# Kernel optimization log

Hardware: AMD Instinct MI355X
Metric: run time of the kernel (lower is better)

The kernel has to match this reference:

```python
import jax, jax.numpy as jnp
import numpy as np

N = 2800        # real node count (before hardcoded pad)
NPAD = 3000     # module pads node dim to 3000
F_IN = 8192     # node_features
H1 = 256        # dim_h1 (GCLSTM in_channels)
H2 = 128        # GCLSTM out_channels
E = 179200      # edges (avg degree 64)


def setup_inputs() -> dict:
    key = jax.random.key(0)
    ks = jax.random.split(key, 12)
    inp = {
        "x": jax.random.normal(ks[0], (N, F_IN), jnp.float32),
        "edge_index": jax.random.randint(ks[1], (2, E), 0, N, dtype=jnp.int64),
        "edge_weight": jax.random.uniform(ks[2], (E,), jnp.float32),
        "h0": jax.random.normal(ks[3], (NPAD, H2), jnp.float32),
        "c0": jax.random.normal(ks[4], (NPAD, H2), jnp.float32),
        # fc0: node_features -> dim_h1
        "fc0_w": jax.random.normal(ks[5], (F_IN, H1), jnp.float32) / np.float32(np.sqrt(F_IN)),
        "fc0_b": jnp.zeros((H1,), jnp.float32),
        # GCLSTM gate params, stacked over gates [i, f, c, o]
        "Wx": jax.random.normal(ks[6], (4, H1, H2), jnp.float32) / np.float32(np.sqrt(H1)),
        "bg": jnp.zeros((4, H2), jnp.float32),
        # ChebConv (K=2) weights per gate: theta_0, theta_1, bias
        "cw0": jax.random.normal(ks[7], (4, H2, H2), jnp.float32) / np.float32(np.sqrt(H2)),
        "cw1": jax.random.normal(ks[8], (4, H2, H2), jnp.float32) / np.float32(np.sqrt(H2)),
        "cb": jnp.zeros((4, H2), jnp.float32),
        # final fc: 128 -> 1
        "fc_w": jax.random.normal(ks[9], (H2, 1), jnp.float32) / np.float32(np.sqrt(H2)),
        "fc_b": jnp.zeros((1,), jnp.float32),
    }
    return inp


def _cheb_scaled_laplacian(edge_index, edge_weight, num_nodes):
    # ChebConv 'sym' norm with lambda_max=2: L_hat = -D^{-1/2} A D^{-1/2}
    # (diagonal of scaled Laplacian cancels to zero with fill_value=-1 self loops)
    row, col = edge_index[0], edge_index[1]
    deg = jax.ops.segment_sum(edge_weight, row, num_segments=num_nodes)
    dinv = jnp.where(deg > 0, jax.lax.rsqrt(jnp.where(deg > 0, deg, 1.0)), 0.0)
    return -dinv[row] * edge_weight * dinv[col]  # per-edge weight of L_hat


def reference(x, edge_weight, h0, c0, fc0_w, fc0_b, Wx, bg, cw0, cw1, cb,
              fc_w, fc_b, edge_index):
    n_real = x.shape[0]
    # hardcoded zero-padding of node dim to 3000
    xp = jnp.concatenate([x, jnp.zeros((NPAD - n_real, x.shape[1]), x.dtype)], axis=0)
    z = jax.nn.relu(xp @ fc0_w + fc0_b)                       # [3000, 256]

    row, col = edge_index[0], edge_index[1]
    w_hat = _cheb_scaled_laplacian(edge_index, edge_weight, NPAD)
    # Chebyshev T1 term: L_hat @ H  (shared across all four gates)
    T1 = jax.ops.segment_sum(w_hat[:, None] * h0[row], col, num_segments=NPAD)  # [3000,128]

    # all four gate pre-activations at once: X W_x + ChebConv(H) + b
    gates = (jnp.einsum('nf,gfo->gno', z, Wx)
             + jnp.einsum('nd,gdo->gno', h0, cw0)
             + jnp.einsum('nd,gdo->gno', T1, cw1)
             + (bg + cb)[:, None, :])                          # [4, 3000, 128]

    i = jax.nn.sigmoid(gates[0])
    f = jax.nn.sigmoid(gates[1])
    t = jnp.tanh(gates[2])
    o = jax.nn.sigmoid(gates[3])
    c_new = f * c0 + i * t
    h_new = o * jnp.tanh(c_new)                                # [3000, 128]

    out = (jax.nn.relu(h_new) @ fc_w + fc_b)[:, 0]             # squeeze last dim
    out = out[:n_real]                                         # drop padding rows
    return out, h_new
```

## Files before the change

kernel.cpp:

```cpp
#include <hip/hip_runtime.h>
#include <math.h>

#define N_REAL 2800
#define NPAD   3000
#define F_IN   8192
#define H1     256
#define H2     128
#define NE     179200
#define UDIM   512
#define NGATE  512
#define MPAD   3072
#define SPLITK 16
#define KCH    (F_IN / SPLITK)

typedef _Float16 half8_t __attribute__((ext_vector_type(8)));
typedef _Float16 half4_t __attribute__((ext_vector_type(4)));
typedef float    floatx4 __attribute__((ext_vector_type(4)));

__device__ __forceinline__ void async_g2l_16(const _Float16* g, _Float16* l) {
    __builtin_amdgcn_global_load_lds(
        (const __attribute__((address_space(1))) unsigned int*)g,
        (__attribute__((address_space(3))) unsigned int*)l, 16, 0, 0);
}

__global__ __launch_bounds__(256)
void prep_kernel(const float* __restrict__ w, const float* __restrict__ Wx,
                 const float* __restrict__ cw0, const float* __restrict__ cw1,
                 const float* __restrict__ bg, const float* __restrict__ cb,
                 _Float16* __restrict__ wT, _Float16* __restrict__ Wc,
                 float* __restrict__ biasv) {
    int b = blockIdx.x;
    if (b < 2048) {
        __shared__ float tile[32][33];
        int k0 = (b & 255) * 32;
        int n0 = (b >> 8) * 32;
        int tx = threadIdx.x & 31, ty = threadIdx.x >> 5;
#pragma unroll
        for (int r = 0; r < 4; r++)
            tile[ty + r * 8][tx] = w[(size_t)(k0 + ty + r * 8) * H1 + n0 + tx];
        __syncthreads();
#pragma unroll
        for (int r = 0; r < 4; r++)
            wT[(size_t)(n0 + ty + r * 8) * F_IN + k0 + tx] = (_Float16)tile[tx][ty + r * 8];
    } else {
        int idx = (b - 2048) * 256 + threadIdx.x;
        if (idx < UDIM * NGATE) {
            int col = idx >> 9;
            int f   = idx & 511;
            int g = col >> 7, o = col & 127;
            float v;
            if (f < H1)            v = Wx[((size_t)g * H1 + f) * H2 + o];
            else if (f < H1 + H2)  v = cw0[((size_t)g * H2 + (f - H1)) * H2 + o];
            else                   v = cw1[((size_t)g * H2 + (f - H1 - H2)) * H2 + o];
            Wc[idx] = (_Float16)v;
            if (f == 0) biasv[col] = bg[col] + cb[col];
        }
    }
}

__global__ __launch_bounds__(256, 3)
void gemm1_fused(const float* __restrict__ x, const _Float16* __restrict__ wT,
                 float* __restrict__ P) {
    __shared__ __align__(16) _Float16 As[8][64][8];
    __shared__ __align__(16) _Float16 Bs[8][256][8];
    const int t = threadIdx.x;
    const int wave = t >> 6, lane = t & 63;
    const int l16 = lane & 15, u4 = lane >> 4;
    const int m0 = blockIdx.x * 64;
    const int kbase = blockIdx.y * KCH;

    const int arow = t >> 2;
    const int aseg = t & 3;
    const bool avalid = (m0 + arow) < N_REAL;
    const float* agp = x + (size_t)(m0 + arow) * F_IN + kbase + aseg * 16;

    floatx4 acc[4][4] = {};

    for (int kk = 0; kk < KCH; kk += 64) {
#pragma unroll
        for (int q = 0; q < 2; q++) {
            int u = wave * 2 + q;
            const _Float16* bsrc = wT + kbase + kk + u * 8;
#pragma unroll
            for (int rg = 0; rg < 4; rg++)
                async_g2l_16(bsrc + (size_t)(rg * 64 + lane) * F_IN, &Bs[u][rg * 64 + lane][0]);
        }
        float4 a0 = make_float4(0.f, 0.f, 0.f, 0.f), a1 = a0, a2 = a0, a3 = a0;
        if (avalid) {
            a0 = *(const float4*)(agp + kk);
            a1 = *(const float4*)(agp + kk + 4);
            a2 = *(const float4*)(agp + kk + 8);
            a3 = *(const float4*)(agp + kk + 12);
        }
        half8_t hlo, hhi;
        hlo[0] = (_Float16)a0.x; hlo[1] = (_Float16)a0.y; hlo[2] = (_Float16)a0.z; hlo[3] = (_Float16)a0.w;
        hlo[4] = (_Float16)a1.x; hlo[5] = (_Float16)a1.y; hlo[6] = (_Float16)a1.z; hlo[7] = (_Float16)a1.w;
        hhi[0] = (_Float16)a2.x; hhi[1] = (_Float16)a2.y; hhi[2] = (_Float16)a2.z; hhi[3] = (_Float16)a2.w;
        hhi[4] = (_Float16)a3.x; hhi[5] = (_Float16)a3.y; hhi[6] = (_Float16)a3.z; hhi[7] = (_Float16)a3.w;
        *(half8_t*)&As[aseg * 2][arow][0]     = hlo;
        *(half8_t*)&As[aseg * 2 + 1][arow][0] = hhi;
        __syncthreads();
#pragma unroll
        for (int ks = 0; ks < 2; ks++) {
            half8_t a[4], b[4];
#pragma unroll
            for (int i = 0; i < 4; i++) a[i] = *(const half8_t*)&As[ks * 4 + u4][i * 16 + l16][0];
#pragma unroll
            for (int j = 0; j < 4; j++) b[j] = *(const half8_t*)&Bs[ks * 4 + u4][wave * 64 + j * 16 + l16][0];
#pragma unroll
            for (int i = 0; i < 4; i++)
#pragma unroll
                for (int j = 0; j < 4; j++)
                    acc[i][j] = __builtin_amdgcn_mfma_f32_16x16x32_f16(a[i], b[j], acc[i][j], 0, 0, 0);
        }
        __syncthreads();
    }

    float* Pb = P + ((size_t)blockIdx.y * MPAD + m0) * H1;
#pragma unroll
    for (int i = 0; i < 4; i++)
#pragma unroll
        for (int j = 0; j < 4; j++) {
            int n = wave * 64 + j * 16 + l16;
#pragma unroll
            for (int r = 0; r < 4; r++)
                Pb[(size_t)(i * 16 + u4 * 4 + r) * H1 + n] = acc[i][j][r];
        }
}

__global__ void hist_kernel(const int* __restrict__ ei, const float* __restrict__ ew,
                            float* __restrict__ deg, int* __restrict__ counts) {
    int e = blockIdx.x * blockDim.x + threadIdx.x;
    if (e < NE) {
        int r = ei[e];
        int c = ei[NE + e];
        atomicAdd(&deg[r], ew[e]);
        atomicAdd(&counts[c], 1);
    }
}

__global__ __launch_bounds__(1024)
void scan_kernel(const int* __restrict__ counts, int* __restrict__ offsets,
                 const float* __restrict__ deg, float* __restrict__ dinv,
                 int* __restrict__ cursor) {
    __shared__ int wt[16];
    int t = threadIdx.x;
    int i0 = t * 3;
    int v0 = (i0     < NPAD) ? counts[i0]     : 0;
    int v1 = (i0 + 1 < NPAD) ? counts[i0 + 1] : 0;
    int v2 = (i0 + 2 < NPAD) ? counts[i0 + 2] : 0;
    int s = v0 + v1 + v2;
    int incl = s;
#pragma unroll
    for (int d = 1; d < 64; d <<= 1) {
        int n = __shfl_up(incl, d);
        if ((t & 63) >= d) incl += n;
    }
    if ((t & 63) == 63) wt[t >> 6] = incl;
    __syncthreads();
    if (t < 64) {
        int w = (t < 16) ? wt[t] : 0;
        int wi = w;
#pragma unroll
        for (int d = 1; d < 16; d <<= 1) {
            int n = __shfl_up(wi, d);
            if (t >= d) wi += n;
        }
        if (t < 16) wt[t] = wi - w;
    }
    __syncthreads();
    int base = wt[t >> 6] + (incl - s);
    if (i0 <= NPAD)     { offsets[i0] = base;              if (i0     < NPAD) cursor[i0]     = base; }
    if (i0 + 1 <= NPAD) { offsets[i0 + 1] = base + v0;     if (i0 + 1 < NPAD) cursor[i0 + 1] = base + v0; }
    if (i0 + 2 <= NPAD) { offsets[i0 + 2] = base + v0 + v1; if (i0 + 2 < NPAD) cursor[i0 + 2] = base + v0 + v1; }
    for (int i = t; i < NPAD; i += 1024) {
        float d = deg[i];
        dinv[i] = (d > 0.f) ? rsqrtf(d) : 0.f;
    }
}

__global__ void scatter_kernel(const int* __restrict__ ei, int* __restrict__ cursor,
                               int* __restrict__ eid) {
    int e = blockIdx.x * blockDim.x + threadIdx.x;
    if (e < NE) {
        int c = ei[NE + e];
        int p = atomicAdd(&cursor[c], 1);
        eid[p] = e;
    }
}

#define ZBLK 1536
#define HBLK 768
__global__ __launch_bounds__(128)
void t1epi_kernel(const int* __restrict__ ei, const float* __restrict__ ew,
                  const float* __restrict__ h0, const float* __restrict__ dinv,
                  const int* __restrict__ offsets, const int* __restrict__ eid,
                  const float* __restrict__ P, const float* __restrict__ fc0_b,
                  _Float16* __restrict__ U16) {
    int b = blockIdx.x;
    int t = threadIdx.x;
    if (b < NPAD) {
        __shared__ int   sr[128];
        __shared__ float sw[128];
        int n = b;
        int beg = offsets[n], end = offsets[n + 1];
        float dc = dinv[n];
        float acc = 0.f;
        for (int base = beg; base < end; base += 128) {
            int j = base + t;
            if (j < end) {
                int e = eid[j];
                int r = ei[e];
                sr[t] = r;
                sw[t] = -dinv[r] * ew[e];
            }
            __syncthreads();
            int cnt = min(128, end - base);
            for (int k = 0; k < cnt; k++)
                acc += sw[k] * h0[(size_t)sr[k] * H2 + t];
            __syncthreads();
        }
        U16[(size_t)n * UDIM + H1 + H2 + t] = (_Float16)(acc * dc);
    } else if (b < NPAD + ZBLK) {
        int q = (b - NPAD) * 128 + t;
        int m = q >> 6;
        int n4 = (q & 63) * 4;
        float sx = 0.f, sy = 0.f, sz = 0.f, sw = 0.f;
#pragma unroll
        for (int sk = 0; sk < SPLITK; sk++) {
            float4 p = *(const float4*)&P[((size_t)sk * MPAD + m) * H1 + n4];
            sx += p.x; sy += p.y; sz += p.z; sw += p.w;
        }
        float4 bb = *(const float4*)&fc0_b[n4];
        half4_t h;
        h[0] = (_Float16)fmaxf(sx + bb.x, 0.f);
        h[1] = (_Float16)fmaxf(sy + bb.y, 0.f);
        h[2] = (_Float16)fmaxf(sz + bb.z, 0.f);
        h[3] = (_Float16)fmaxf(sw + bb.w, 0.f);
        *(half4_t*)&U16[(size_t)m * UDIM + n4] = h;
    } else {
        int q = (b - NPAD - ZBLK) * 128 + t;
        int m = q >> 5;
        int o4 = (q & 31) * 4;
        half4_t h = {};
        if (m < NPAD) {
            float4 v = *(const float4*)&h0[(size_t)m * H2 + o4];
            h[0] = (_Float16)v.x; h[1] = (_Float16)v.y; h[2] = (_Float16)v.z; h[3] = (_Float16)v.w;
        }
        *(half4_t*)&U16[(size_t)m * UDIM + H1 + o4] = h;
    }
}

__global__ __launch_bounds__(256, 3)
void gemm2_mfma(const _Float16* __restrict__ U16, const _Float16* __restrict__ Wc,
                float* __restrict__ gates) {
    __shared__ __align__(16) _Float16 As[8][64][8];
    __shared__ __align__(16) _Float16 Bs[8][256][8];
    const int t = threadIdx.x;
    const int wave = t >> 6, lane = t & 63;
    const int l16 = lane & 15, u4 = lane >> 4;
    const int n0 = blockIdx.x * 256;
    const int m0 = blockIdx.y * 64;

    floatx4 acc[4][4] = {};

    for (int kk = 0; kk < UDIM; kk += 64) {
#pragma unroll
        for (int q = 0; q < 2; q++) {
            int u = wave * 2 + q;
            async_g2l_16(U16 + (size_t)(m0 + lane) * UDIM + kk + u * 8, &As[u][lane][0]);
            const _Float16* bsrc = Wc + kk + u * 8;
#pragma unroll
            for (int rg = 0; rg < 4; rg++)
                async_g2l_16(bsrc + (size_t)(n0 + rg * 64 + lane) * UDIM, &Bs[u][rg * 64 + lane][0]);
        }
        __syncthreads();
#pragma unroll
        for (int ks = 0; ks < 2; ks++) {
            half8_t a[4], b[4];
#pragma unroll
            for (int i = 0; i < 4; i++) a[i] = *(const half8_t*)&As[ks * 4 + u4][i * 16 + l16][0];
#pragma unroll
            for (int j = 0; j < 4; j++) b[j] = *(const half8_t*)&Bs[ks * 4 + u4][wave * 64 + j * 16 + l16][0];
#pragma unroll
            for (int i = 0; i < 4; i++)
#pragma unroll
                for (int j = 0; j < 4; j++)
                    acc[i][j] = __builtin_amdgcn_mfma_f32_16x16x32_f16(a[i], b[j], acc[i][j], 0, 0, 0);
        }
        __syncthreads();
    }

#pragma unroll
    for (int i = 0; i < 4; i++)
#pragma unroll
        for (int j = 0; j < 4; j++) {
            int n = n0 + wave * 64 + j * 16 + l16;
#pragma unroll
            for (int r = 0; r < 4; r++)
                gates[(size_t)(m0 + i * 16 + u4 * 4 + r) * NGATE + n] = acc[i][j][r];
        }
}

__global__ __launch_bounds__(128)
void lstm_kernel(const float* __restrict__ gates, const float* __restrict__ c0,
                 const float* __restrict__ biasv, const float* __restrict__ fc_w,
                 const float* __restrict__ fc_b, float* __restrict__ out) {
    __shared__ float red[2];
    int n = blockIdx.x;
    int o = threadIdx.x;
    const float* g = gates + (size_t)n * NGATE;
    float gi = g[o]          + biasv[o];
    float gf = g[H2 + o]     + biasv[H2 + o];
    float gt = g[2 * H2 + o] + biasv[2 * H2 + o];
    float go = g[3 * H2 + o] + biasv[3 * H2 + o];
    float iv = 1.f / (1.f + expf(-gi));
    float fv = 1.f / (1.f + expf(-gf));
    float tv = tanhf(gt);
    float ov = 1.f / (1.f + expf(-go));
    float c = fv * c0[(size_t)n * H2 + o] + iv * tv;
    float h = ov * tanhf(c);
    out[N_REAL + (size_t)n * H2 + o] = h;

    float r = fmaxf(h, 0.f) * fc_w[o];
#pragma unroll
    for (int s = 32; s; s >>= 1) r += __shfl_down(r, s);
    if ((o & 63) == 0) red[o >> 6] = r;
    __syncthreads();
    if (o == 0 && n < N_REAL) out[n] = red[0] + red[1] + fc_b[0];
}

extern "C" void kernel_launch(void* const* d_in, const int* in_sizes, int n_in,
                              void* d_out, int out_size, void* d_ws, size_t ws_size,
                              hipStream_t stream) {
    const float* x     = (const float*)d_in[0];
    const int*   ei    = (const int*)d_in[1];
    const float* ew    = (const float*)d_in[2];
    const float* h0    = (const float*)d_in[3];
    const float* c0    = (const float*)d_in[4];
    const float* fc0_w = (const float*)d_in[5];
    const float* fc0_b = (const float*)d_in[6];
    const float* Wx    = (const float*)d_in[7];
    const float* bg    = (const float*)d_in[8];
    const float* cw0   = (const float*)d_in[9];
    const float* cw1   = (const float*)d_in[10];
    const float* cb    = (const float*)d_in[11];
    const float* fc_w  = (const float*)d_in[12];
    const float* fc_b  = (const float*)d_in[13];
    float* out = (float*)d_out;

    float* P      = (float*)d_ws;
    float* gates  = P + (size_t)SPLITK * MPAD * H1;
    float* biasv  = gates + (size_t)MPAD * NGATE;
    float* deg    = biasv + NGATE;
    float* dinv   = deg + NPAD;
    int*   counts = (int*)(dinv + NPAD);
    int*   offs   = counts + 3072;
    int*   cursor = offs + 3072;
    int*   eid    = cursor + 3072;
    _Float16* U16 = (_Float16*)(((uintptr_t)(eid + NE) + 255) & ~(uintptr_t)255);
    _Float16* Wc  = U16 + (size_t)MPAD * UDIM;
    _Float16* wT  = Wc + (size_t)UDIM * NGATE;

    hipMemsetAsync(deg, 0, NPAD * sizeof(float), stream);
    hipMemsetAsync(counts, 0, 3072 * sizeof(int), stream);

    prep_kernel<<<3072, 256, 0, stream>>>(fc0_w, Wx, cw0, cw1, bg, cb, wT, Wc, biasv);
    gemm1_fused<<<dim3(MPAD / 64, SPLITK), 256, 0, stream>>>(x, wT, P);
    hist_kernel<<<(NE + 255) / 256, 256, 0, stream>>>(ei, ew, deg, counts);
    scan_kernel<<<1, 1024, 0, stream>>>(counts, offs, deg, dinv, cursor);
    scatter_kernel<<<(NE + 255) / 256, 256, 0, stream>>>(ei, cursor, eid);
    t1epi_kernel<<<NPAD + ZBLK + HBLK, 128, 0, stream>>>(ei, ew, h0, dinv, offs, eid, P, fc0_b, U16);
    gemm2_mfma<<<dim3(NGATE / 256, MPAD / 64), 256, 0, stream>>>(U16, Wc, gates);
    lstm_kernel<<<NPAD, 128, 0, stream>>>(gates, c0, biasv, fc_w, fc_b, out);
}
```

Baseline: 295.7 us.

## Store split-K partials in fp16, split gemm2 K, unroll T1 gather, fold memsets

The gemm1 split-K partial sums are now written and read as fp16 instead of fp32, halving the partial-buffer traffic, and gemm1's launch bounds are raised to 4 blocks per SM. gemm2 gets a 2-way K split, writing two partial gate buffers that the LSTM kernel adds together, so it launches twice as many blocks. The T1 neighbour gather is unrolled by 8 to keep more loads in flight. The two memsets are folded into extra prep_kernel blocks to save launches. Rounding partials to fp16 before the reduction adds precision risk.

```diff
diff --git a/kernel.cpp b/kernel.cpp
--- a/kernel.cpp
+++ b/kernel.cpp
@@ -28,7 +28,8 @@
                  const float* __restrict__ cw0, const float* __restrict__ cw1,
                  const float* __restrict__ bg, const float* __restrict__ cb,
                  _Float16* __restrict__ wT, _Float16* __restrict__ Wc,
-                 float* __restrict__ biasv) {
+                 float* __restrict__ biasv, float* __restrict__ deg,
+                 int* __restrict__ counts) {
     int b = blockIdx.x;
     if (b < 2048) {
         __shared__ float tile[32][33];
@@ -42,7 +43,7 @@
 #pragma unroll
         for (int r = 0; r < 4; r++)
             wT[(size_t)(n0 + ty + r * 8) * F_IN + k0 + tx] = (_Float16)tile[tx][ty + r * 8];
-    } else {
+    } else if (b < 3072) {
         int idx = (b - 2048) * 256 + threadIdx.x;
         if (idx < UDIM * NGATE) {
             int col = idx >> 9;
@@ -55,12 +56,16 @@
             Wc[idx] = (_Float16)v;
             if (f == 0) biasv[col] = bg[col] + cb[col];
         }
-    }
-}
-
-__global__ __launch_bounds__(256, 3)
+    } else {
+        int i = (b - 3072) * 256 + threadIdx.x;
+        if (i < NPAD) deg[i] = 0.f;
+        else { int j = i - NPAD; if (j < 3072) counts[j] = 0; }
+    }
+}
+
+__global__ __launch_bounds__(256, 4)
 void gemm1_fused(const float* __restrict__ x, const _Float16* __restrict__ wT,
-                 float* __restrict__ P) {
+                 _Float16* __restrict__ P) {
     __shared__ __align__(16) _Float16 As[8][64][8];
     __shared__ __align__(16) _Float16 Bs[8][256][8];
     const int t = threadIdx.x;
@@ -116,7 +121,7 @@
         __syncthreads();
     }
 
-    float* Pb = P + ((size_t)blockIdx.y * MPAD + m0) * H1;
+    _Float16* Pb = P + ((size_t)blockIdx.y * MPAD + m0) * H1;
 #pragma unroll
     for (int i = 0; i < 4; i++)
 #pragma unroll
@@ -124,7 +129,7 @@
             int n = wave * 64 + j * 16 + l16;
 #pragma unroll
             for (int r = 0; r < 4; r++)
-                Pb[(size_t)(i * 16 + u4 * 4 + r) * H1 + n] = acc[i][j][r];
+                Pb[(size_t)(i * 16 + u4 * 4 + r) * H1 + n] = (_Float16)acc[i][j][r];
         }
 }
 
@@ -170,8 +175,8 @@
     }
     __syncthreads();
     int base = wt[t >> 6] + (incl - s);
-    if (i0 <= NPAD)     { offsets[i0] = base;              if (i0     < NPAD) cursor[i0]     = base; }
-    if (i0 + 1 <= NPAD) { offsets[i0 + 1] = base + v0;     if (i0 + 1 < NPAD) cursor[i0 + 1] = base + v0; }
+    if (i0 <= NPAD)     { offsets[i0] = base;               if (i0     < NPAD) cursor[i0]     = base; }
+    if (i0 + 1 <= NPAD) { offsets[i0 + 1] = base + v0;      if (i0 + 1 < NPAD) cursor[i0 + 1] = base + v0; }
     if (i0 + 2 <= NPAD) { offsets[i0 + 2] = base + v0 + v1; if (i0 + 2 < NPAD) cursor[i0 + 2] = base + v0 + v1; }
     for (int i = t; i < NPAD; i += 1024) {
         float d = deg[i];
@@ -195,7 +200,7 @@
 void t1epi_kernel(const int* __restrict__ ei, const float* __restrict__ ew,
                   const float* __restrict__ h0, const float* __restrict__ dinv,
                   const int* __restrict__ offsets, const int* __restrict__ eid,
-                  const float* __restrict__ P, const float* __restrict__ fc0_b,
+                  const _Float16* __restrict__ P, const float* __restrict__ fc0_b,
                   _Float16* __restrict__ U16) {
     int b = blockIdx.x;
     int t = threadIdx.x;
@@ -216,7 +221,24 @@
             }
             __syncthreads();
             int cnt = min(128, end - base);
-            for (int k = 0; k < cnt; k++)
+            int k = 0;
+            for (; k + 8 <= cnt; k += 8) {
+                int   r0 = sr[k],   r1 = sr[k+1], r2 = sr[k+2], r3 = sr[k+3];
+                int   r4 = sr[k+4], r5 = sr[k+5], r6 = sr[k+6], r7 = sr[k+7];
+                float w0 = sw[k],   w1 = sw[k+1], w2 = sw[k+2], w3 = sw[k+3];
+                float w4 = sw[k+4], w5 = sw[k+5], w6 = sw[k+6], w7 = sw[k+7];
+                float v0 = h0[(size_t)r0 * H2 + t];
+                float v1 = h0[(size_t)r1 * H2 + t];
+                float v2 = h0[(size_t)r2 * H2 + t];
+                float v3 = h0[(size_t)r3 * H2 + t];
+                float v4 = h0[(size_t)r4 * H2 + t];
+                float v5 = h0[(size_t)r5 * H2 + t];
+                float v6 = h0[(size_t)r6 * H2 + t];
+                float v7 = h0[(size_t)r7 * H2 + t];
+                acc += w0 * v0 + w1 * v1 + w2 * v2 + w3 * v3
+                     + w4 * v4 + w5 * v5 + w6 * v6 + w7 * v7;
+            }
+            for (; k < cnt; k++)
                 acc += sw[k] * h0[(size_t)sr[k] * H2 + t];
             __syncthreads();
         }
@@ -225,18 +247,18 @@
         int q = (b - NPAD) * 128 + t;
         int m = q >> 6;
         int n4 = (q & 63) * 4;
-        float sx = 0.f, sy = 0.f, sz = 0.f, sw = 0.f;
+        float s0 = 0.f, s1 = 0.f, s2 = 0.f, s3 = 0.f;
 #pragma unroll
         for (int sk = 0; sk < SPLITK; sk++) {
-            float4 p = *(const float4*)&P[((size_t)sk * MPAD + m) * H1 + n4];
-            sx += p.x; sy += p.y; sz += p.z; sw += p.w;
+            half4_t p = *(const half4_t*)&P[((size_t)sk * MPAD + m) * H1 + n4];
+            s0 += (float)p[0]; s1 += (float)p[1]; s2 += (float)p[2]; s3 += (float)p[3];
         }
         float4 bb = *(const float4*)&fc0_b[n4];
         half4_t h;
-        h[0] = (_Float16)fmaxf(sx + bb.x, 0.f);
-        h[1] = (_Float16)fmaxf(sy + bb.y, 0.f);
-        h[2] = (_Float16)fmaxf(sz + bb.z, 0.f);
-        h[3] = (_Float16)fmaxf(sw + bb.w, 0.f);
+        h[0] = (_Float16)fmaxf(s0 + bb.x, 0.f);
+        h[1] = (_Float16)fmaxf(s1 + bb.y, 0.f);
+        h[2] = (_Float16)fmaxf(s2 + bb.z, 0.f);
+        h[3] = (_Float16)fmaxf(s3 + bb.w, 0.f);
         *(half4_t*)&U16[(size_t)m * UDIM + n4] = h;
     } else {
         int q = (b - NPAD - ZBLK) * 128 + t;
@@ -253,7 +275,7 @@
 
 __global__ __launch_bounds__(256, 3)
 void gemm2_mfma(const _Float16* __restrict__ U16, const _Float16* __restrict__ Wc,
-                float* __restrict__ gates) {
+                float* __restrict__ gatesP) {
     __shared__ __align__(16) _Float16 As[8][64][8];
     __shared__ __align__(16) _Float16 Bs[8][256][8];
     const int t = threadIdx.x;
@@ -261,10 +283,11 @@
     const int l16 = lane & 15, u4 = lane >> 4;
     const int n0 = blockIdx.x * 256;
     const int m0 = blockIdx.y * 64;
+    const int kz = blockIdx.z * 256;
 
     floatx4 acc[4][4] = {};
 
-    for (int kk = 0; kk < UDIM; kk += 64) {
+    for (int kk = kz; kk < kz + 256; kk += 64) {
 #pragma unroll
         for (int q = 0; q < 2; q++) {
             int u = wave * 2 + q;
@@ -291,6 +314,7 @@
         __syncthreads();
     }
 
+    float* g = gatesP + (size_t)blockIdx.z * MPAD * NGATE;
 #pragma unroll
     for (int i = 0; i < 4; i++)
 #pragma unroll
@@ -298,7 +322,7 @@
             int n = n0 + wave * 64 + j * 16 + l16;
 #pragma unroll
             for (int r = 0; r < 4; r++)
-                gates[(size_t)(m0 + i * 16 + u4 * 4 + r) * NGATE + n] = acc[i][j][r];
+                g[(size_t)(m0 + i * 16 + u4 * 4 + r) * NGATE + n] = acc[i][j][r];
         }
 }
 
@@ -309,11 +333,12 @@
     __shared__ float red[2];
     int n = blockIdx.x;
     int o = threadIdx.x;
-    const float* g = gates + (size_t)n * NGATE;
-    float gi = g[o]          + biasv[o];
-    float gf = g[H2 + o]     + biasv[H2 + o];
-    float gt = g[2 * H2 + o] + biasv[2 * H2 + o];
-    float go = g[3 * H2 + o] + biasv[3 * H2 + o];
+    const float* g0 = gates + (size_t)n * NGATE;
+    const float* g1 = g0 + (size_t)MPAD * NGATE;
+    float gi = g0[o]          + g1[o]          + biasv[o];
+    float gf = g0[H2 + o]     + g1[H2 + o]     + biasv[H2 + o];
+    float gt = g0[2 * H2 + o] + g1[2 * H2 + o] + biasv[2 * H2 + o];
+    float go = g0[3 * H2 + o] + g1[3 * H2 + o] + biasv[3 * H2 + o];
     float iv = 1.f / (1.f + expf(-gi));
     float fv = 1.f / (1.f + expf(-gf));
     float tv = tanhf(gt);
@@ -349,9 +374,9 @@
     const float* fc_b  = (const float*)d_in[13];
     float* out = (float*)d_out;
 
-    float* P      = (float*)d_ws;
-    float* gates  = P + (size_t)SPLITK * MPAD * H1;
-    float* biasv  = gates + (size_t)MPAD * NGATE;
+    _Float16* P   = (_Float16*)d_ws;
+    float* gates  = (float*)(P + (size_t)SPLITK * MPAD * H1);
+    float* biasv  = gates + 2 * (size_t)MPAD * NGATE;
     float* deg    = biasv + NGATE;
     float* dinv   = deg + NPAD;
     int*   counts = (int*)(dinv + NPAD);
@@ -362,15 +387,12 @@
     _Float16* Wc  = U16 + (size_t)MPAD * UDIM;
     _Float16* wT  = Wc + (size_t)UDIM * NGATE;
 
-    hipMemsetAsync(deg, 0, NPAD * sizeof(float), stream);
-    hipMemsetAsync(counts, 0, 3072 * sizeof(int), stream);
-
-    prep_kernel<<<3072, 256, 0, stream>>>(fc0_w, Wx, cw0, cw1, bg, cb, wT, Wc, biasv);
+    prep_kernel<<<3096, 256, 0, stream>>>(fc0_w, Wx, cw0, cw1, bg, cb, wT, Wc, biasv, deg, counts);
     gemm1_fused<<<dim3(MPAD / 64, SPLITK), 256, 0, stream>>>(x, wT, P);
     hist_kernel<<<(NE + 255) / 256, 256, 0, stream>>>(ei, ew, deg, counts);
     scan_kernel<<<1, 1024, 0, stream>>>(counts, offs, deg, dinv, cursor);
     scatter_kernel<<<(NE + 255) / 256, 256, 0, stream>>>(ei, cursor, eid);
     t1epi_kernel<<<NPAD + ZBLK + HBLK, 128, 0, stream>>>(ei, ew, h0, dinv, offs, eid, P, fc0_b, U16);
-    gemm2_mfma<<<dim3(NGATE / 256, MPAD / 64), 256, 0, stream>>>(U16, Wc, gates);
+    gemm2_mfma<<<dim3(NGATE / 256, MPAD / 64, 2), 256, 0, stream>>>(U16, Wc, gates);
     lstm_kernel<<<NPAD, 128, 0, stream>>>(gates, c0, biasv, fc_w, fc_b, out);
 }
```

New measurement: 306.3 us. 1.04x slower.
